# Kernel tuning notes

Hardware: AMD Instinct MI355X
Metric: run time of the kernel (lower is better)

Reference implementation:

```python
import jax, jax.numpy as jnp
import numpy as np
import math

D = 768
H = 8
DH = D // H
T = 4
MODES = 16
NUM_CLASSES = 14


def setup_inputs() -> dict:
    key = jax.random.key(0)
    ks = iter(jax.random.split(key, 64))
    B, S = 256, 512
    inp = {}
    inp['x_feat'] = jax.random.normal(next(ks), (B, S, D), dtype=jnp.float32)
    # attention pool
    inp['pool_w'] = jax.random.normal(next(ks), (D, 1), dtype=jnp.float32) * 0.02
    inp['pool_b'] = jnp.zeros((1,), dtype=jnp.float32)
    # per-block params, stacked over T
    def pstack(shape, scale=0.02):
        return jax.random.normal(next(ks), (T,) + shape, dtype=jnp.float32) * scale
    inp['w_q'] = pstack((D, D)); inp['w_k'] = pstack((D, D)); inp['w_v'] = pstack((D, D))
    inp['b_qkv'] = jnp.zeros((T, 3 * D), dtype=jnp.float32)
    inp['w_o'] = pstack((D, D)); inp['b_o'] = jnp.zeros((T, D), dtype=jnp.float32)
    inp['ln1_g'] = jnp.ones((T, D), dtype=jnp.float32); inp['ln1_b'] = jnp.zeros((T, D), dtype=jnp.float32)
    inp['ln2_g'] = jnp.ones((T, D), dtype=jnp.float32); inp['ln2_b'] = jnp.zeros((T, D), dtype=jnp.float32)
    inp['scale_real'] = pstack((MODES, D)); inp['scale_imag'] = pstack((MODES, D))
    inp['proj_w'] = pstack((D, D)); inp['proj_b'] = jnp.zeros((T, D), dtype=jnp.float32)
    inp['bn_g'] = jnp.ones((T, D), dtype=jnp.float32); inp['bn_b'] = jnp.zeros((T, D), dtype=jnp.float32)
    inp['gate'] = jnp.full((T,), 0.5, dtype=jnp.float32)
    inp['scale_attn'] = jnp.ones((T,), dtype=jnp.float32)
    inp['scale_denoise'] = jnp.ones((T,), dtype=jnp.float32)
    # fuse MLP + classifier
    inp['f1_w'] = jax.random.normal(next(ks), (D, 256), dtype=jnp.float32) * 0.02
    inp['f1_b'] = jnp.zeros((256,), dtype=jnp.float32)
    inp['f1_bn_g'] = jnp.ones((256,), dtype=jnp.float32); inp['f1_bn_b'] = jnp.zeros((256,), dtype=jnp.float32)
    inp['f2_w'] = jax.random.normal(next(ks), (256, 128), dtype=jnp.float32) * 0.02
    inp['f2_b'] = jnp.zeros((128,), dtype=jnp.float32)
    inp['f2_bn_g'] = jnp.ones((128,), dtype=jnp.float32); inp['f2_bn_b'] = jnp.zeros((128,), dtype=jnp.float32)
    inp['cls_w'] = jax.random.normal(next(ks), (128, NUM_CLASSES), dtype=jnp.float32) * 0.02
    inp['cls_b'] = jnp.zeros((NUM_CLASSES,), dtype=jnp.float32)
    return inp


def _layernorm(x, g, b, eps=1e-5):
    mu = jnp.mean(x, axis=-1, keepdims=True)
    var = jnp.var(x, axis=-1, keepdims=True)
    return (x - mu) * jax.lax.rsqrt(var + eps) * g + b


def _bn_eval(x, g, b, eps=1e-5):
    # eval-mode BatchNorm1d with running_mean=0, running_var=1
    return x * (g / jnp.sqrt(1.0 + eps)) + b


def _forward(x_feat, pool_w, pool_b, w_q, w_k, w_v, b_qkv, w_o, b_o,
             ln1_g, ln1_b, ln2_g, ln2_b, scale_real, scale_imag, proj_w, proj_b,
             bn_g, bn_b, gate, scale_attn, scale_denoise,
             f1_w, f1_b, f1_bn_g, f1_bn_b, f2_w, f2_b, f2_bn_g, f2_bn_b,
             cls_w, cls_b):
    B, S, _ = x_feat.shape
    # attention pool: softmax over seq of a scalar score per token
    scores = x_feat @ pool_w + pool_b          # [B,S,1]
    weights = jax.nn.softmax(scores, axis=1)
    z = jnp.sum(weights * x_feat, axis=1)      # [B,D]

    def classify(z):
        h = jax.nn.relu(_bn_eval(z @ f1_w + f1_b, f1_bn_g, f1_bn_b))
        h = jax.nn.relu(_bn_eval(h @ f2_w + f2_b, f2_bn_g, f2_bn_b))
        return h @ cls_w + cls_b

    logits_sum = jnp.zeros((B, NUM_CLASSES), dtype=x_feat.dtype)
    for t in range(T):
        bq, bk, bv = b_qkv[t, :D], b_qkv[t, D:2 * D], b_qkv[t, 2 * D:]
        # query: single token z [B,1,D]; keys/values: x_feat [B,S,D]
        q = (z @ w_q[t].T + bq).reshape(B, H, 1, DH)
        k = (x_feat @ w_k[t].T + bk).reshape(B, S, H, DH).transpose(0, 2, 1, 3)
        v = (x_feat @ w_v[t].T + bv).reshape(B, S, H, DH).transpose(0, 2, 1, 3)
        att = jax.nn.softmax(jnp.einsum('bhqd,bhsd->bhqs', q, k) / math.sqrt(DH), axis=-1)
        o = jnp.einsum('bhqs,bhsd->bhqd', att, v).reshape(B, D)
        z_attn = o @ w_o[t].T + b_o[t]
        z1 = _layernorm(z + scale_attn[t] * z_attn, ln1_g[t], ln1_b[t])
        # fft denoise: keep first MODES freq bins scaled by mean of complex filter per mode
        z_freq = jnp.fft.fft(z1, axis=1)                        # [B,D] complex
        filt = jnp.mean(scale_real[t] + 1j * scale_imag[t], axis=1)  # [MODES] complex
        keep = z_freq[:, :MODES] * filt[None, :]
        z_filtered = jnp.concatenate([keep, jnp.zeros((B, D - MODES), dtype=z_freq.dtype)], axis=1)
        z_spatial = jnp.fft.ifft(z_filtered, axis=1).real
        z_den = z_spatial @ proj_w[t].T + proj_b[t]
        z2 = _layernorm(z1 + scale_denoise[t] * z_den, ln2_g[t], ln2_b[t])
        g = jax.nn.sigmoid(gate[t])
        z3 = g * z2 + (1.0 - g) * z
        z = _bn_eval(z3, bn_g[t], bn_b[t])
        logits_sum = logits_sum + classify(z)
    return logits_sum / T


def reference(x_feat, pool_w, pool_b, w_q, w_k, w_v, b_qkv, w_o, b_o,
              ln1_g, ln1_b, ln2_g, ln2_b, scale_real, scale_imag, proj_w, proj_b,
              bn_g, bn_b, gate, scale_attn, scale_denoise,
              f1_w, f1_b, f1_bn_g, f1_bn_b, f2_w, f2_b, f2_bn_g, f2_bn_b,
              cls_w, cls_b):
    return _forward(x_feat, pool_w, pool_b, w_q, w_k, w_v, b_qkv, w_o, b_o,
                    ln1_g, ln1_b, ln2_g, ln2_b, scale_real, scale_imag, proj_w, proj_b,
                    bn_g, bn_b, gate, scale_attn, scale_denoise,
                    f1_w, f1_b, f1_bn_g, f1_bn_b, f2_w, f2_b, f2_bn_g, f2_bn_b,
                    cls_w, cls_b)
```

## Files before the change

### kernel.cpp

```cpp
#include <hip/hip_runtime.h>
#include <math.h>


#define DEV __device__ __forceinline__

typedef unsigned int   uint32;
typedef unsigned short ushort_t;
typedef __attribute__((ext_vector_type(8))) short bf16x8;
typedef __attribute__((ext_vector_type(4))) float f32x4;
typedef __attribute__((ext_vector_type(2))) float f32x2;

constexpr int Bv  = 256;
constexpr int Sv  = 512;
constexpr int Dv  = 768;
constexpr int Hv  = 8;
constexpr int DHv = 96;
constexpr int NCv = 14;

constexpr size_t ZL  = 196608;
constexpr size_t XWL = 1572864;
constexpr size_t WL  = 2359296;
constexpr size_t WT  = 589824;

DEV float4 ld4(const float* p) { return *reinterpret_cast<const float4*>(p); }

DEV ushort_t f2bf(float f) {
    uint32 u = __float_as_uint(f);
    u += 0x7FFFu + ((u >> 16) & 1u);
    return (ushort_t)(u >> 16);
}
DEV float bf2f(ushort_t h) { return __uint_as_float((uint32)h << 16); }
DEV void split2(float f, ushort_t& hi, ushort_t& lo) {
    hi = f2bf(f);
    lo = f2bf(f - bf2f(hi));
}
DEV uint2 pack4(float4 v) {
    return make_uint2((uint32)f2bf(v.x) | ((uint32)f2bf(v.y) << 16),
                      (uint32)f2bf(v.z) | ((uint32)f2bf(v.w) << 16));
}

DEV f32x2 bfpair(uint32 u) {
    f32x2 r;
    r.x = __uint_as_float(u << 16);
    r.y = __uint_as_float(u & 0xFFFF0000u);
    return r;
}

DEV f32x2 pkfma(f32x2 a, f32x2 b, f32x2 c) {
    f32x2 d;
    asm("v_pk_fma_f32 %0, %1, %2, %3" : "=v"(d) : "v"(a), "v"(b), "v"(c));
    return d;
}

DEV void glds16(const void* g, void* l) {
    __builtin_amdgcn_global_load_lds(
        (const __attribute__((address_space(1))) void*)g,
        (__attribute__((address_space(3))) void*)l, 16, 0, 0);
}

__global__ __launch_bounds__(512, 4)
void pool_cvt_kernel(const float* __restrict__ x, const float* __restrict__ pool_w,
                     ushort_t* __restrict__ xbf,
                     float* __restrict__ pacc, float2* __restrict__ pml)
{
    __shared__ float qks[Dv];
    const int b = blockIdx.x, half = blockIdx.y;
    const int tid = threadIdx.x, wave = tid >> 6, lane = tid & 63;
    for (int i = tid; i < Dv / 4; i += 512)
        *reinterpret_cast<float4*>(&qks[i * 4]) = ld4(pool_w + i * 4);
    __syncthreads();

    const int row0 = half * 256 + wave * 32;
    const float* base = x + ((size_t)b * Sv + row0) * Dv + 4 * lane;

    float4 acc[3];
#pragma unroll
    for (int j = 0; j < 3; ++j) acc[j] = make_float4(0.f, 0.f, 0.f, 0.f);
    float m = -INFINITY, l = 0.f;

    float4 c0[3], c1[3];
#pragma unroll
    for (int j = 0; j < 3; ++j) { c0[j] = ld4(base + 256 * j); c1[j] = ld4(base + Dv + 256 * j); }

    for (int it = 0; it < 16; ++it) {
        float4 n0_[3], n1_[3];
        if (it < 15) {
            const float* nb = base + (size_t)(2 * it + 2) * Dv;
#pragma unroll
            for (int j = 0; j < 3; ++j) { n0_[j] = ld4(nb + 256 * j); n1_[j] = ld4(nb + Dv + 256 * j); }
        }
        ushort_t* ob = xbf + ((size_t)b * Sv + row0 + 2 * it) * Dv + 4 * lane;
#pragma unroll
        for (int j = 0; j < 3; ++j) *reinterpret_cast<uint2*>(ob + 256 * j) = pack4(c0[j]);
#pragma unroll
        for (int j = 0; j < 3; ++j) *reinterpret_cast<uint2*>(ob + Dv + 256 * j) = pack4(c1[j]);
        float p0 = 0.f, p1 = 0.f;
#pragma unroll
        for (int j = 0; j < 3; ++j) {
            const float4 q4 = *reinterpret_cast<const float4*>(&qks[4 * lane + 256 * j]);
            p0 = fmaf(q4.x, c0[j].x, p0); p0 = fmaf(q4.y, c0[j].y, p0);
            p0 = fmaf(q4.z, c0[j].z, p0); p0 = fmaf(q4.w, c0[j].w, p0);
            p1 = fmaf(q4.x, c1[j].x, p1); p1 = fmaf(q4.y, c1[j].y, p1);
            p1 = fmaf(q4.z, c1[j].z, p1); p1 = fmaf(q4.w, c1[j].w, p1);
        }
#pragma unroll
        for (int dd = 1; dd < 64; dd <<= 1) { p0 += __shfl_xor(p0, dd); p1 += __shfl_xor(p1, dd); }
        float mx = fmaxf(p0, p1);
        if (mx > m) {
            float r = __expf(m - mx); l *= r;
#pragma unroll
            for (int j = 0; j < 3; ++j) { acc[j].x *= r; acc[j].y *= r; acc[j].z *= r; acc[j].w *= r; }
            m = mx;
        }
        float w0 = __expf(p0 - m), w1 = __expf(p1 - m);
        l += w0 + w1;
#pragma unroll
        for (int j = 0; j < 3; ++j) {
            acc[j].x = fmaf(w1, c1[j].x, fmaf(w0, c0[j].x, acc[j].x));
            acc[j].y = fmaf(w1, c1[j].y, fmaf(w0, c0[j].y, acc[j].y));
            acc[j].z = fmaf(w1, c1[j].z, fmaf(w0, c0[j].z, acc[j].z));
            acc[j].w = fmaf(w1, c1[j].w, fmaf(w0, c0[j].w, acc[j].w));
        }
        if (it < 15) {
#pragma unroll
            for (int j = 0; j < 3; ++j) { c0[j] = n0_[j]; c1[j] = n1_[j]; }
        }
    }
    const int p = half * 8 + wave;
    const size_t pidx = (size_t)p * 256 + b;
#pragma unroll
    for (int j = 0; j < 3; ++j)
        *reinterpret_cast<float4*>(&pacc[pidx * Dv + 4 * lane + 256 * j]) = acc[j];
    if (lane == 0) pml[pidx] = make_float2(m, l);
}

__global__ __launch_bounds__(512, 4)
void attn_flash_kernel(const ushort_t* __restrict__ xbf, const float* __restrict__ Qk,
                       float* __restrict__ pacc, float2* __restrict__ pml, float scale)
{
    const int b = blockIdx.x, half = blockIdx.y;
    const int tid = threadIdx.x, wave = tid >> 6, lane = tid & 63;
    const int hg = wave & 3, slice = wave >> 2;
    const int h0 = 2 * hg, h1 = h0 + 1;
    const int row0 = half * 256 + slice * 128;

    f32x2 q0[6], q1[6];
    {
        const float* qp0 = Qk + ((size_t)b * Hv + h0) * Dv + 4 * lane;
        const float* qp1 = Qk + ((size_t)b * Hv + h1) * Dv + 4 * lane;
#pragma unroll
        for (int s = 0; s < 3; ++s) {
            float4 a = ld4(qp0 + s * 256);
            float4 c = ld4(qp1 + s * 256);
            q0[2 * s]     = (f32x2){a.x, a.y}; q0[2 * s + 1] = (f32x2){a.z, a.w};
            q1[2 * s]     = (f32x2){c.x, c.y}; q1[2 * s + 1] = (f32x2){c.z, c.w};
        }
    }
    f32x2 a0[6], a1[6];
#pragma unroll
    for (int c = 0; c < 6; ++c) { a0[c] = (f32x2){0.f, 0.f}; a1[c] = (f32x2){0.f, 0.f}; }
    float m0 = -INFINITY, l0 = 0.f, m1 = -INFINITY, l1 = 0.f;

    const ushort_t* base = xbf + ((size_t)b * Sv + row0) * Dv + 4 * lane;

    uint2 c0[3], c1[3];
#pragma unroll
    for (int s = 0; s < 3; ++s) {
        c0[s] = *reinterpret_cast<const uint2*>(base + s * 256);
        c1[s] = *reinterpret_cast<const uint2*>(base + Dv + s * 256);
    }

    for (int it = 0; it < 64; ++it) {
        uint2 n0[3], n1[3];
        if (it < 63) {
            const ushort_t* nb = base + (size_t)(2 * it + 2) * Dv;
#pragma unroll
            for (int s = 0; s < 3; ++s) {
                n0[s] = *reinterpret_cast<const uint2*>(nb + s * 256);
                n1[s] = *reinterpret_cast<const uint2*>(nb + Dv + s * 256);
            }
        }
        f32x2 xf0[6], xf1[6];
#pragma unroll
        for (int s = 0; s < 3; ++s) {
            xf0[2 * s] = bfpair(c0[s].x); xf0[2 * s + 1] = bfpair(c0[s].y);
            xf1[2 * s] = bfpair(c1[s].x); xf1[2 * s + 1] = bfpair(c1[s].y);
        }
        f32x2 t00 = (f32x2){0.f, 0.f}, t01 = t00, t10 = t00, t11 = t00;
#pragma unroll
        for (int c = 0; c < 6; ++c) {
            t00 = pkfma(xf0[c], q0[c], t00);
            t01 = pkfma(xf0[c], q1[c], t01);
            t10 = pkfma(xf1[c], q0[c], t10);
            t11 = pkfma(xf1[c], q1[c], t11);
        }
        float s4[4];
        s4[0] = t00.x + t00.y;
        s4[1] = t01.x + t01.y;
        s4[2] = t10.x + t10.y;
        s4[3] = t11.x + t11.y;
        {
            const bool k0 = (lane & 1), k1 = (lane & 2);
            float sd0 = k0 ? s4[0] : s4[1];
            float rc0 = __shfl_xor(sd0, 1);
            float t0  = (k0 ? s4[1] : s4[0]) + rc0;
            float sd1 = k0 ? s4[2] : s4[3];
            float rc1 = __shfl_xor(sd1, 1);
            float t1  = (k0 ? s4[3] : s4[2]) + rc1;
            float sd2 = k1 ? t0 : t1;
            float rc2 = __shfl_xor(sd2, 2);
            float u   = (k1 ? t1 : t0) + rc2;
            u += __shfl_xor(u, 4);  u += __shfl_xor(u, 8);
            u += __shfl_xor(u, 16); u += __shfl_xor(u, 32);
            float b1 = __shfl_xor(u, 1);
            float b2 = __shfl_xor(u, 2);
            float b3 = __shfl_xor(u, 3);
            s4[0] = k1 ? (k0 ? b3 : b2) : (k0 ? b1 : u);
            s4[1] = k1 ? (k0 ? b2 : b3) : (k0 ? u  : b1);
            s4[2] = k1 ? (k0 ? b1 : u ) : (k0 ? b3 : b2);
            s4[3] = k1 ? (k0 ? u  : b1) : (k0 ? b2 : b3);
        }
#pragma unroll
        for (int j = 0; j < 4; ++j) s4[j] *= scale;
        {
            float mx = fmaxf(s4[0], s4[2]);
            if (mx > m0) {
                float f = __expf(m0 - mx); l0 *= f;
#pragma unroll
                for (int c = 0; c < 6; ++c) { a0[c].x *= f; a0[c].y *= f; }
                m0 = mx;
            }
            float w0 = __expf(s4[0] - m0), w1 = __expf(s4[2] - m0);
            l0 += w0 + w1;
            f32x2 w02 = (f32x2){w0, w0}, w12 = (f32x2){w1, w1};
#pragma unroll
            for (int c = 0; c < 6; ++c) a0[c] = pkfma(xf1[c], w12, pkfma(xf0[c], w02, a0[c]));
        }
        {
            float mx = fmaxf(s4[1], s4[3]);
            if (mx > m1) {
                float f = __expf(m1 - mx); l1 *= f;
#pragma unroll
                for (int c = 0; c < 6; ++c) { a1[c].x *= f; a1[c].y *= f; }
                m1 = mx;
            }
            float w0 = __expf(s4[1] - m1), w1 = __expf(s4[3] - m1);
            l1 += w0 + w1;
            f32x2 w02 = (f32x2){w0, w0}, w12 = (f32x2){w1, w1};
#pragma unroll
            for (int c = 0; c < 6; ++c) a1[c] = pkfma(xf1[c], w12, pkfma(xf0[c], w02, a1[c]));
        }
        if (it < 63) {
#pragma unroll
            for (int s = 0; s < 3; ++s) { c0[s] = n0[s]; c1[s] = n1[s]; }
        }
    }

    const int p = half * 2 + slice;
    const size_t pidx0 = ((size_t)p * 256 + b) * Hv + h0;
    const size_t pidx1 = pidx0 + 1;
    float* pb0 = pacc + pidx0 * Dv + 4 * lane;
    float* pb1 = pacc + pidx1 * Dv + 4 * lane;
#pragma unroll
    for (int s = 0; s < 3; ++s) {
        *reinterpret_cast<float4*>(pb0 + s * 256) =
            make_float4(a0[2 * s].x, a0[2 * s].y, a0[2 * s + 1].x, a0[2 * s + 1].y);
        *reinterpret_cast<float4*>(pb1 + s * 256) =
            make_float4(a1[2 * s].x, a1[2 * s].y, a1[2 * s + 1].x, a1[2 * s + 1].y);
    }
    if (lane == 0) {
        pml[pidx0] = make_float2(m0, l0);
        pml[pidx1] = make_float2(m1, l1);
    }
}

template<int NH, int NP, bool WF32>
__global__ __launch_bounds__(256)
void merge_kernel(const float* __restrict__ pacc, const float2* __restrict__ pml,
                  ushort_t* __restrict__ obf, size_t loOff, float* __restrict__ of32)
{
    __shared__ float eS[NH * NP];
    const int b = blockIdx.x, tid = threadIdx.x;
    if (tid < NH) {
        float2 mls[NP];
        float mm = -INFINITY;
#pragma unroll
        for (int p = 0; p < NP; ++p) {
            mls[p] = pml[((size_t)p * 256 + b) * NH + tid];
            mm = fmaxf(mm, mls[p].x);
        }
        float ee[NP]; float L = 0.f;
#pragma unroll
        for (int p = 0; p < NP; ++p) { ee[p] = __expf(mls[p].x - mm); L += mls[p].y * ee[p]; }
        float inv = 1.f / L;
#pragma unroll
        for (int p = 0; p < NP; ++p) eS[tid * NP + p] = ee[p] * inv;
    }
    __syncthreads();
#pragma unroll
    for (int seg = 0; seg < NH * 3; ++seg) {
        int h = seg / 3;
        int d = (seg - h * 3) * 256 + tid;
        float v = 0.f;
#pragma unroll
        for (int p = 0; p < NP; ++p)
            v += pacc[((size_t)((size_t)p * 256 + b) * NH + h) * Dv + d] * eS[h * NP + p];
        size_t oi = ((size_t)b * NH + h) * Dv + d;
        ushort_t hi, lo; split2(v, hi, lo);
        obf[oi] = hi; obf[oi + loOff] = lo;
        if (WF32) of32[oi] = v;
    }
}

template<int MODE, bool OBF>
__global__ __launch_bounds__(256)
void mgemm_kernel(const ushort_t* __restrict__ A, size_t aLo,
                  const ushort_t* __restrict__ W, size_t wLo,
                  const float* __restrict__ bias, void* __restrict__ outp,
                  size_t oLo)
{
    constexpr int BN = (MODE == 2) ? 96 : 64;
    constexpr int BK = (MODE == 1) ? 32 : 64;
    constexpr int NJ = BN / 32;
    constexpr int KTOT = (MODE == 1) ? 96 : 768;
    constexpr int NSTEP = KTOT / BK;
    constexpr int CH = BK / 8;
    constexpr int CA = (64 * BK) / 512;
    constexpr int CB = (BN * BK) / 512;
    constexpr int NC = 2 * (CA + CB) / 4;
    constexpr int LDA = (MODE == 2) ? 6144 : 768;
    constexpr int LDW = (MODE == 1) ? 96 : 768;
    constexpr int LDO = (MODE == 1) ? 6144 : 768;
    constexpr int WCW = (MODE == 2) ? 48 : 32;
    constexpr int RSH = (BK == 64) ? 7 : 6;

    __shared__ ushort_t As[2][2][64 * BK];
    __shared__ ushort_t Bs[2][2][BN * BK];

    const int tid = threadIdx.x, wave = tid >> 6, lane = tid & 63;
    const int n0 = blockIdx.x * BN;
    const int m0 = blockIdx.y * 64;
    const int h  = (MODE == 1) ? blockIdx.z : ((MODE == 2) ? blockIdx.x : 0);
    const int acol = (MODE == 1) ? h * 96 : ((MODE == 2) ? h * 768 : 0);
    const ushort_t* Wb = W + ((MODE == 1) ? (size_t)h * 768 * 96 : (size_t)0);
    const int ocol = (MODE == 1) ? h * 768 : 0;

    const int wr = wave >> 1, wc = wave & 1;
    const int l15 = lane & 15, kg = lane >> 4;

    auto stage = [&](int kt, int buf) {
#pragma unroll
        for (int hl = 0; hl < 2; ++hl) {
            const ushort_t* Ap = A + (hl ? aLo : 0);
            const ushort_t* Wp = Wb + (hl ? wLo : 0);
#pragma unroll
            for (int c = 0; c < CA / 4; ++c) {
                int call = wave + 4 * c;
                int off = call * 1024 + lane * 16;
                int row = off >> RSH;
                int chunk = (off & (2 * BK - 1)) >> 4;
                int sw = chunk ^ (row & (CH - 1));
                const ushort_t* src = Ap + (size_t)(m0 + row) * LDA + acol + kt + sw * 8;
                glds16(src, (char*)As[buf][hl] + call * 1024);
            }
#pragma unroll
            for (int c = 0; c < CB / 4; ++c) {
                int call = wave + 4 * c;
                int off = call * 1024 + lane * 16;
                int row = off >> RSH;
                int chunk = (off & (2 * BK - 1)) >> 4;
                int sw = chunk ^ (row & (CH - 1));
                const ushort_t* src = Wp + (size_t)(n0 + row) * LDW + kt + sw * 8;
                glds16(src, (char*)Bs[buf][hl] + call * 1024);
            }
        }
    };

    f32x4 acc[2][NJ];
#pragma unroll
    for (int i = 0; i < 2; ++i)
#pragma unroll
        for (int j = 0; j < NJ; ++j) acc[i][j] = (f32x4){0.f, 0.f, 0.f, 0.f};

    stage(0, 0);
    int cur = 0;
    for (int s = 0; s < NSTEP; ++s) {
        __builtin_amdgcn_s_barrier();
        if (s + 1 < NSTEP) {
            stage((s + 1) * BK, cur ^ 1);
            asm volatile("s_waitcnt vmcnt(%0)" :: "i"(NC) : "memory");
        } else {
            asm volatile("s_waitcnt vmcnt(0)" ::: "memory");
        }
        __builtin_amdgcn_s_barrier();
        __builtin_amdgcn_sched_barrier(0);

        const ushort_t* ah_ = As[cur][0];
        const ushort_t* al_ = As[cur][1];
        const ushort_t* bh_ = Bs[cur][0];
        const ushort_t* bl_ = Bs[cur][1];
#pragma unroll
        for (int kw = 0; kw < BK / 32; ++kw) {
            const int kb = kw * 4;
            bf16x8 ah[2], al[2], bh[NJ], bl[NJ];
#pragma unroll
            for (int i = 0; i < 2; ++i) {
                int r = wr * 32 + i * 16 + l15;
                int c = (kb + kg) ^ (r & (CH - 1));
                ah[i] = *reinterpret_cast<const bf16x8*>(&ah_[r * BK + c * 8]);
                al[i] = *reinterpret_cast<const bf16x8*>(&al_[r * BK + c * 8]);
            }
#pragma unroll
            for (int j = 0; j < NJ; ++j) {
                int r = wc * WCW + j * 16 + l15;
                int c = (kb + kg) ^ (r & (CH - 1));
                bh[j] = *reinterpret_cast<const bf16x8*>(&bh_[r * BK + c * 8]);
                bl[j] = *reinterpret_cast<const bf16x8*>(&bl_[r * BK + c * 8]);
            }
#pragma unroll
            for (int i = 0; i < 2; ++i)
#pragma unroll
                for (int j = 0; j < NJ; ++j) {
                    acc[i][j] = __builtin_amdgcn_mfma_f32_16x16x32_bf16(al[i], bh[j], acc[i][j], 0, 0, 0);
                    acc[i][j] = __builtin_amdgcn_mfma_f32_16x16x32_bf16(ah[i], bl[j], acc[i][j], 0, 0, 0);
                    acc[i][j] = __builtin_amdgcn_mfma_f32_16x16x32_bf16(ah[i], bh[j], acc[i][j], 0, 0, 0);
                }
        }
        cur ^= 1;
    }

#pragma unroll
    for (int i = 0; i < 2; ++i)
#pragma unroll
        for (int j = 0; j < NJ; ++j) {
            int rg = m0 + wr * 32 + i * 16 + kg * 4;
            int cg = n0 + wc * WCW + j * 16 + l15;
            float bv = bias ? bias[cg] : 0.f;
#pragma unroll
            for (int reg = 0; reg < 4; ++reg) {
                float v = acc[i][j][reg] + bv;
                size_t oi = (size_t)(rg + reg) * LDO + ocol + cg;
                if (OBF) {
                    ushort_t hi, lo; split2(v, hi, lo);
                    ((ushort_t*)outp)[oi] = hi;
                    ((ushort_t*)outp)[oi + oLo] = lo;
                } else {
                    ((float*)outp)[oi] = v;
                }
            }
        }
}

__global__ __launch_bounds__(256)
void cvt3_kernel(const float* __restrict__ wq, const float* __restrict__ wv,
                 const float* __restrict__ wo, ushort_t* __restrict__ dst)
{
    const int bid = blockIdx.x;
    const int w = bid / 1152;
    const int off = (bid - w * 1152) * 2048 + threadIdx.x * 8;
    const float* src = (w == 0) ? wq : (w == 1) ? wv : wo;
    ushort_t hi[8], lo[8];
#pragma unroll
    for (int e = 0; e < 8; ++e) split2(src[off + e], hi[e], lo[e]);
    ushort_t* base = dst + (size_t)w * (2 * WL);
    *reinterpret_cast<uint4*>(base + off) = *reinterpret_cast<uint4*>(hi);
    *reinterpret_cast<uint4*>(base + WL + off) = *reinterpret_cast<uint4*>(lo);
}

__global__ __launch_bounds__(256)
void wkT_kernel(const float* __restrict__ w_k, ushort_t* __restrict__ wkT)
{
    __shared__ float tile[96][65];
    const int n0 = blockIdx.x * 64;
    const int th = blockIdx.y;
    const int t = th >> 3, h = th & 7;
    const float* src = w_k + ((size_t)t * Dv + h * DHv) * Dv + n0;
    for (int idx = threadIdx.x; idx < 96 * 64; idx += 256) {
        int j = idx >> 6, n = idx & 63;
        tile[j][n] = src[(size_t)j * Dv + n];
    }
    __syncthreads();
    for (int idx = threadIdx.x; idx < 64 * 96; idx += 256) {
        int n = idx / 96, j = idx - n * 96;
        ushort_t hi, lo; split2(tile[j][n], hi, lo);
        size_t oi = ((size_t)th * Dv + n0 + n) * DHv + j;
        wkT[oi] = hi; wkT[oi + WL] = lo;
    }
}

__global__ __launch_bounds__(256)
void pre1_kernel(float* __restrict__ twc, float* __restrict__ tws,
                 const float* __restrict__ sr, const float* __restrict__ si,
                 float* __restrict__ filt)
{
    __shared__ float red[8];
    const int bid = blockIdx.x;
    if (bid < 48) {
        int idx = bid * 256 + threadIdx.x;
        int k = idx / Dv, n = idx % Dv;
        int r = (k * n) % Dv;
        float ang = (float)r * (float)(6.283185307179586 / 768.0);
        twc[idx] = cosf(ang);
        tws[idx] = sinf(ang);
    } else {
        int tk = bid - 48;
        const float* a  = sr + (size_t)tk * Dv;
        const float* b2 = si + (size_t)tk * Dv;
        float s1 = 0.f, s2 = 0.f;
#pragma unroll
        for (int j = 0; j < 3; ++j) {
            int c = threadIdx.x + 256 * j;
            s1 += a[c]; s2 += b2[c];
        }
        int wave = threadIdx.x >> 6, lane = threadIdx.x & 63;
#pragma unroll
        for (int dd = 1; dd < 64; dd <<= 1) { s1 += __shfl_xor(s1, dd); s2 += __shfl_xor(s2, dd); }
        if (lane == 0) { red[wave * 2] = s1; red[wave * 2 + 1] = s2; }
        __syncthreads();
        if (threadIdx.x == 0) {
            filt[tk * 2]     = (red[0] + red[2] + red[4] + red[6]) * (1.f / 768.f);
            filt[tk * 2 + 1] = (red[1] + red[3] + red[5] + red[7]) * (1.f / 768.f);
        }
    }
}

__global__ __launch_bounds__(256)
void cs_kernel(const float* __restrict__ proj_w, const float* __restrict__ twc,
               const float* __restrict__ tws, float* __restrict__ csC,
               float* __restrict__ csS)
{
    const int wave = threadIdx.x >> 6, lane = threadIdx.x & 63;
    const int gw = blockIdx.x * 4 + wave;
    const int t = gw / 768;
    const int i = gw - t * 768;
    const float* pr = proj_w + ((size_t)t * Dv + i) * Dv + 4 * lane;
    float4 p4[3];
#pragma unroll
    for (int j = 0; j < 3; ++j) p4[j] = ld4(pr + 256 * j);
    for (int k = 0; k < 16; ++k) {
        const float* tc = twc + (size_t)k * Dv + 4 * lane;
        const float* ts = tws + (size_t)k * Dv + 4 * lane;
        float ac = 0.f, as = 0.f;
#pragma unroll
        for (int j = 0; j < 3; ++j) {
            float4 c4 = ld4(tc + 256 * j);
            float4 s4 = ld4(ts + 256 * j);
            ac = fmaf(p4[j].x, c4.x, ac); ac = fmaf(p4[j].y, c4.y, ac);
            ac = fmaf(p4[j].z, c4.z, ac); ac = fmaf(p4[j].w, c4.w, ac);
            as = fmaf(p4[j].x, s4.x, as); as = fmaf(p4[j].y, s4.y, as);
            as = fmaf(p4[j].z, s4.z, as); as = fmaf(p4[j].w, s4.w, as);
        }
#pragma unroll
        for (int dd = 1; dd < 64; dd <<= 1) {
            ac += __shfl_xor(ac, dd);
            as += __shfl_xor(as, dd);
        }
        if (lane == 0) {
            csC[((size_t)t * 16 + k) * Dv + i] = ac * (1.f / 768.f);
            csS[((size_t)t * 16 + k) * Dv + i] = as * (1.f / 768.f);
        }
    }
}

__global__ __launch_bounds__(256)
void lnden_kernel(float* __restrict__ z, ushort_t* __restrict__ zbf,
                  const float* __restrict__ za,
                  const float* __restrict__ g1, const float* __restrict__ b1,
                  const float* __restrict__ g2, const float* __restrict__ b2,
                  const float* __restrict__ bng, const float* __restrict__ bnb,
                  const float* __restrict__ gate_p, const float* __restrict__ sa_p,
                  const float* __restrict__ sd_p,
                  const float* __restrict__ twc, const float* __restrict__ tws,
                  const float* __restrict__ filt_t,
                  const float* __restrict__ csC_t, const float* __restrict__ csS_t,
                  const float* __restrict__ pb_t,
                  const float* __restrict__ f1w, const float* __restrict__ f1b,
                  const float* __restrict__ f1g, const float* __restrict__ f1bb,
                  const float* __restrict__ f2w, const float* __restrict__ f2b,
                  const float* __restrict__ f2g, const float* __restrict__ f2bb,
                  const float* __restrict__ clw, const float* __restrict__ clb,
                  float* __restrict__ outp, int t)
{
    const int b = blockIdx.x, tid = threadIdx.x;
    const int wave = tid >> 6, lane = tid & 63;
    __shared__ float red[8];
    __shared__ float dred[4][32];
    __shared__ float fin[32];
    __shared__ float kr[16], ki[16];
    __shared__ float zs[768];
    __shared__ float h1s[256];
    __shared__ float h2s[128];

    const float sa = sa_p[0];
    float v[3], zo[3];
    float s = 0.f, s2 = 0.f;
#pragma unroll
    for (int j = 0; j < 3; ++j) {
        int c = tid + 256 * j;
        zo[j] = z[(size_t)b * Dv + c];
        float val = zo[j] + sa * za[(size_t)b * Dv + c];
        v[j] = val; s += val; s2 += val * val;
    }
#pragma unroll
    for (int dd = 1; dd < 64; dd <<= 1) { s += __shfl_xor(s, dd); s2 += __shfl_xor(s2, dd); }
    if (lane == 0) { red[wave * 2] = s; red[wave * 2 + 1] = s2; }
    __syncthreads();
    {
        const float mean = (red[0] + red[2] + red[4] + red[6]) * (1.f / 768.f);
        const float var  = (red[1] + red[3] + red[5] + red[7]) * (1.f / 768.f) - mean * mean;
        const float rstd = rsqrtf(var + 1e-5f);
#pragma unroll
        for (int j = 0; j < 3; ++j) {
            int c = tid + 256 * j;
            v[j] = (v[j] - mean) * rstd * g1[c] + b1[c];
        }
    }
    float Fc[16], Fs[16];
#pragma unroll
    for (int k = 0; k < 16; ++k) { Fc[k] = 0.f; Fs[k] = 0.f; }
#pragma unroll
    for (int j = 0; j < 3; ++j) {
        int c = tid + 256 * j;
#pragma unroll
        for (int k = 0; k < 16; ++k) {
            Fc[k] = fmaf(v[j], twc[k * Dv + c], Fc[k]);
            Fs[k] = fmaf(v[j], tws[k * Dv + c], Fs[k]);
        }
    }
#pragma unroll
    for (int dd = 1; dd < 64; dd <<= 1) {
#pragma unroll
        for (int k = 0; k < 16; ++k) { Fc[k] += __shfl_xor(Fc[k], dd); Fs[k] += __shfl_xor(Fs[k], dd); }
    }
    if (lane == 0) {
#pragma unroll
        for (int k = 0; k < 16; ++k) { dred[wave][k] = Fc[k]; dred[wave][16 + k] = Fs[k]; }
    }
    __syncthreads();
    if (tid < 32) fin[tid] = dred[0][tid] + dred[1][tid] + dred[2][tid] + dred[3][tid];
    __syncthreads();
    if (tid < 16) {
        float Sc = fin[tid], Ss = fin[16 + tid];
        float fr = filt_t[tid * 2], fi = filt_t[tid * 2 + 1];
        kr[tid] = Sc * fr + Ss * fi;
        ki[tid] = Sc * fi - Ss * fr;
    }
    __syncthreads();

    const float sd  = sd_p[0];
    const float gv  = 1.f / (1.f + expf(-gate_p[0]));
    const float bnc = 1.f / sqrtf(1.f + 1e-5f);
    float w3[3];
    s = 0.f; s2 = 0.f;
#pragma unroll
    for (int j = 0; j < 3; ++j) {
        int c = tid + 256 * j;
        float den = pb_t[c];
#pragma unroll
        for (int k = 0; k < 16; ++k) {
            den = fmaf(kr[k], csC_t[k * Dv + c], den);
            den = fmaf(-ki[k], csS_t[k * Dv + c], den);
        }
        float val = v[j] + sd * den;
        w3[j] = val; s += val; s2 += val * val;
    }
#pragma unroll
    for (int dd = 1; dd < 64; dd <<= 1) { s += __shfl_xor(s, dd); s2 += __shfl_xor(s2, dd); }
    if (lane == 0) { red[wave * 2] = s; red[wave * 2 + 1] = s2; }
    __syncthreads();
    const float mean2 = (red[0] + red[2] + red[4] + red[6]) * (1.f / 768.f);
    const float var2  = (red[1] + red[3] + red[5] + red[7]) * (1.f / 768.f) - mean2 * mean2;
    const float rstd2 = rsqrtf(var2 + 1e-5f);
#pragma unroll
    for (int j = 0; j < 3; ++j) {
        int c = tid + 256 * j;
        float z2v = (w3[j] - mean2) * rstd2 * g2[c] + b2[c];
        float z3v = gv * z2v + (1.f - gv) * zo[j];
        float zn  = z3v * (bng[c] * bnc) + bnb[c];
        z[(size_t)b * Dv + c] = zn;
        ushort_t hi, lo; split2(zn, hi, lo);
        zbf[(size_t)b * Dv + c] = hi;
        zbf[(size_t)b * Dv + c + ZL] = lo;
        zs[c] = zn;
    }
    __syncthreads();
    float h = f1b[tid];
    for (int d = 0; d < 768; ++d) h = fmaf(zs[d], f1w[(size_t)d * 256 + tid], h);
    h = h * (f1g[tid] * bnc) + f1bb[tid];
    h1s[tid] = fmaxf(h, 0.f);
    __syncthreads();
    if (tid < 128) {
        float h2 = f2b[tid];
        for (int i2 = 0; i2 < 256; ++i2) h2 = fmaf(h1s[i2], f2w[(size_t)i2 * 128 + tid], h2);
        h2 = h2 * (f2g[tid] * bnc) + f2bb[tid];
        h2s[tid] = fmaxf(h2, 0.f);
    }
    __syncthreads();
    if (tid < NCv) {
        float lg = clb[tid];
        for (int i2 = 0; i2 < 128; ++i2) lg = fmaf(h2s[i2], clw[(size_t)i2 * NCv + tid], lg);
        lg *= 0.25f;
        if (t == 0) outp[(size_t)b * NCv + tid] = lg;
        else        outp[(size_t)b * NCv + tid] += lg;
    }
}

extern "C" void kernel_launch(void* const* d_in, const int* in_sizes, int n_in,
                              void* d_out, int out_size, void* d_ws, size_t ws_size,
                              hipStream_t stream)
{
    (void)in_sizes; (void)n_in; (void)out_size; (void)ws_size;
    const float* x      = (const float*)d_in[0];
    const float* pool_w = (const float*)d_in[1];
    const float* w_q   = (const float*)d_in[3];
    const float* w_k   = (const float*)d_in[4];
    const float* w_v   = (const float*)d_in[5];
    const float* b_qkv = (const float*)d_in[6];
    const float* w_o   = (const float*)d_in[7];
    const float* b_o   = (const float*)d_in[8];
    const float* ln1_g = (const float*)d_in[9];
    const float* ln1_b = (const float*)d_in[10];
    const float* ln2_g = (const float*)d_in[11];
    const float* ln2_b = (const float*)d_in[12];
    const float* s_re  = (const float*)d_in[13];
    const float* s_im  = (const float*)d_in[14];
    const float* proj_w= (const float*)d_in[15];
    const float* proj_b= (const float*)d_in[16];
    const float* bn_g  = (const float*)d_in[17];
    const float* bn_b  = (const float*)d_in[18];
    const float* gate  = (const float*)d_in[19];
    const float* s_at  = (const float*)d_in[20];
    const float* s_dn  = (const float*)d_in[21];
    const float* f1w   = (const float*)d_in[22];
    const float* f1b   = (const float*)d_in[23];
    const float* f1g   = (const float*)d_in[24];
    const float* f1bb  = (const float*)d_in[25];
    const float* f2w   = (const float*)d_in[26];
    const float* f2b   = (const float*)d_in[27];
    const float* f2g   = (const float*)d_in[28];
    const float* f2bb  = (const float*)d_in[29];
    const float* clw   = (const float*)d_in[30];
    const float* clb   = (const float*)d_in[31];
    float* out = (float*)d_out;

    float* ws   = (float*)d_ws;
    float* twc  = ws;
    float* tws  = twc + 12288;
    float* filt = tws + 12288;
    float* csC  = filt + 128;
    float* csS  = csC + 49152;
    float* z    = csS + 49152;
    float* za   = z + 196608;
    float* Qk   = za + 196608;
    float* pacc = Qk + 1572864;
    float* pmlf = pacc + 6291456;
    ushort_t* xbf  = (ushort_t*)(pmlf + 16384);
    ushort_t* zbf  = xbf + 100663296;
    ushort_t* qbf  = zbf + 2 * ZL;
    ushort_t* xwbf = qbf + 2 * ZL;
    ushort_t* obf  = xwbf + 2 * XWL;
    ushort_t* wspl = obf + 2 * ZL;
    ushort_t* wkT  = wspl + 6 * WL;
    float2* pml = (float2*)pmlf;
    ushort_t* wqbf = wspl;
    ushort_t* wvbf = wspl + 2 * WL;
    ushort_t* wobf = wspl + 4 * WL;

    pre1_kernel<<<112, 256, 0, stream>>>(twc, tws, s_re, s_im, filt);
    cs_kernel<<<768, 256, 0, stream>>>(proj_w, twc, tws, csC, csS);
    cvt3_kernel<<<3456, 256, 0, stream>>>(w_q, w_v, w_o, wspl);
    wkT_kernel<<<dim3(12, 32), 256, 0, stream>>>(w_k, wkT);

    pool_cvt_kernel<<<dim3(256, 2), 512, 0, stream>>>(x, pool_w, xbf, pacc, pml);
    merge_kernel<1, 16, true><<<256, 256, 0, stream>>>(pacc, pml, zbf, ZL, z);

    const float iscale = (float)(1.0 / sqrt(96.0));
    for (int t = 0; t < 4; ++t) {
        mgemm_kernel<0, true><<<dim3(12, 4), 256, 0, stream>>>(
            zbf, ZL, wqbf + (size_t)t * WT, WL, b_qkv + (size_t)t * 2304, qbf, ZL);
        mgemm_kernel<1, false><<<dim3(12, 4, 8), 256, 0, stream>>>(
            qbf, ZL, wkT + (size_t)t * WT, WL, nullptr, Qk, 0);
        attn_flash_kernel<<<dim3(256, 2), 512, 0, stream>>>(xbf, Qk, pacc, pml, iscale);
        merge_kernel<8, 4, false><<<256, 256, 0, stream>>>(pacc, pml, xwbf, XWL, nullptr);
        mgemm_kernel<2, true><<<dim3(8, 4), 256, 0, stream>>>(
            xwbf, XWL, wvbf + (size_t)t * WT, WL, b_qkv + (size_t)t * 2304 + 1536, obf, ZL);
        mgemm_kernel<0, false><<<dim3(12, 4), 256, 0, stream>>>(
            obf, ZL, wobf + (size_t)t * WT, WL, b_o + (size_t)t * Dv, za, 0);
        lnden_kernel<<<256, 256, 0, stream>>>(
            z, zbf, za,
            ln1_g + (size_t)t * Dv, ln1_b + (size_t)t * Dv,
            ln2_g + (size_t)t * Dv, ln2_b + (size_t)t * Dv,
            bn_g + (size_t)t * Dv, bn_b + (size_t)t * Dv,
            gate + t, s_at + t, s_dn + t,
            twc, tws, filt + (size_t)t * 32,
            csC + (size_t)t * 12288, csS + (size_t)t * 12288,
            proj_b + (size_t)t * Dv,
            f1w, f1b, f1g, f1bb, f2w, f2b, f2g, f2bb,
            clw, clb, out, t);
    }
}
```

Measured before the change: 930.9 us.

## Split fused flash attention into MFMA score GEMM, softmax, and PV passes

Replaces the single-pass online-softmax attention kernel with three stages: an MFMA bf16 GEMM computing scores from split hi/lo Qk against x, a separate softmax kernel writing bf16 probabilities, and a PV kernel doing only weighted accumulation, followed by a simple sum merge. The aim is to move the QK dot products off packed FMA onto matrix cores and remove the cross-lane shuffle reductions and rescaling from the inner loop. In exchange, x is read twice per step from memory, there are extra launches and intermediate buffers, and probabilities are rounded to bf16.

```diff
diff --git a/kernel.cpp b/kernel.cpp
--- a/kernel.cpp
+++ b/kernel.cpp
@@ -21,6 +21,7 @@
 constexpr size_t XWL = 1572864;
 constexpr size_t WL  = 2359296;
 constexpr size_t WT  = 589824;
+constexpr size_t QKL = 3145728;
 
 DEV float4 ld4(const float* p) { return *reinterpret_cast<const float4*>(p); }
 
@@ -134,146 +135,6 @@
     if (lane == 0) pml[pidx] = make_float2(m, l);
 }
 
-__global__ __launch_bounds__(512, 4)
-void attn_flash_kernel(const ushort_t* __restrict__ xbf, const float* __restrict__ Qk,
-                       float* __restrict__ pacc, float2* __restrict__ pml, float scale)
-{
-    const int b = blockIdx.x, half = blockIdx.y;
-    const int tid = threadIdx.x, wave = tid >> 6, lane = tid & 63;
-    const int hg = wave & 3, slice = wave >> 2;
-    const int h0 = 2 * hg, h1 = h0 + 1;
-    const int row0 = half * 256 + slice * 128;
-
-    f32x2 q0[6], q1[6];
-    {
-        const float* qp0 = Qk + ((size_t)b * Hv + h0) * Dv + 4 * lane;
-        const float* qp1 = Qk + ((size_t)b * Hv + h1) * Dv + 4 * lane;
-#pragma unroll
-        for (int s = 0; s < 3; ++s) {
-            float4 a = ld4(qp0 + s * 256);
-            float4 c = ld4(qp1 + s * 256);
-            q0[2 * s]     = (f32x2){a.x, a.y}; q0[2 * s + 1] = (f32x2){a.z, a.w};
-            q1[2 * s]     = (f32x2){c.x, c.y}; q1[2 * s + 1] = (f32x2){c.z, c.w};
-        }
-    }
-    f32x2 a0[6], a1[6];
-#pragma unroll
-    for (int c = 0; c < 6; ++c) { a0[c] = (f32x2){0.f, 0.f}; a1[c] = (f32x2){0.f, 0.f}; }
-    float m0 = -INFINITY, l0 = 0.f, m1 = -INFINITY, l1 = 0.f;
-
-    const ushort_t* base = xbf + ((size_t)b * Sv + row0) * Dv + 4 * lane;
-
-    uint2 c0[3], c1[3];
-#pragma unroll
-    for (int s = 0; s < 3; ++s) {
-        c0[s] = *reinterpret_cast<const uint2*>(base + s * 256);
-        c1[s] = *reinterpret_cast<const uint2*>(base + Dv + s * 256);
-    }
-
-    for (int it = 0; it < 64; ++it) {
-        uint2 n0[3], n1[3];
-        if (it < 63) {
-            const ushort_t* nb = base + (size_t)(2 * it + 2) * Dv;
-#pragma unroll
-            for (int s = 0; s < 3; ++s) {
-                n0[s] = *reinterpret_cast<const uint2*>(nb + s * 256);
-                n1[s] = *reinterpret_cast<const uint2*>(nb + Dv + s * 256);
-            }
-        }
-        f32x2 xf0[6], xf1[6];
-#pragma unroll
-        for (int s = 0; s < 3; ++s) {
-            xf0[2 * s] = bfpair(c0[s].x); xf0[2 * s + 1] = bfpair(c0[s].y);
-            xf1[2 * s] = bfpair(c1[s].x); xf1[2 * s + 1] = bfpair(c1[s].y);
-        }
-        f32x2 t00 = (f32x2){0.f, 0.f}, t01 = t00, t10 = t00, t11 = t00;
-#pragma unroll
-        for (int c = 0; c < 6; ++c) {
-            t00 = pkfma(xf0[c], q0[c], t00);
-            t01 = pkfma(xf0[c], q1[c], t01);
-            t10 = pkfma(xf1[c], q0[c], t10);
-            t11 = pkfma(xf1[c], q1[c], t11);
-        }
-        float s4[4];
-        s4[0] = t00.x + t00.y;
-        s4[1] = t01.x + t01.y;
-        s4[2] = t10.x + t10.y;
-        s4[3] = t11.x + t11.y;
-        {
-            const bool k0 = (lane & 1), k1 = (lane & 2);
-            float sd0 = k0 ? s4[0] : s4[1];
-            float rc0 = __shfl_xor(sd0, 1);
-            float t0  = (k0 ? s4[1] : s4[0]) + rc0;
-            float sd1 = k0 ? s4[2] : s4[3];
-            float rc1 = __shfl_xor(sd1, 1);
-            float t1  = (k0 ? s4[3] : s4[2]) + rc1;
-            float sd2 = k1 ? t0 : t1;
-            float rc2 = __shfl_xor(sd2, 2);
-            float u   = (k1 ? t1 : t0) + rc2;
-            u += __shfl_xor(u, 4);  u += __shfl_xor(u, 8);
-            u += __shfl_xor(u, 16); u += __shfl_xor(u, 32);
-            float b1 = __shfl_xor(u, 1);
-            float b2 = __shfl_xor(u, 2);
-            float b3 = __shfl_xor(u, 3);
-            s4[0] = k1 ? (k0 ? b3 : b2) : (k0 ? b1 : u);
-            s4[1] = k1 ? (k0 ? b2 : b3) : (k0 ? u  : b1);
-            s4[2] = k1 ? (k0 ? b1 : u ) : (k0 ? b3 : b2);
-            s4[3] = k1 ? (k0 ? u  : b1) : (k0 ? b2 : b3);
-        }
-#pragma unroll
-        for (int j = 0; j < 4; ++j) s4[j] *= scale;
-        {
-            float mx = fmaxf(s4[0], s4[2]);
-            if (mx > m0) {
-                float f = __expf(m0 - mx); l0 *= f;
-#pragma unroll
-                for (int c = 0; c < 6; ++c) { a0[c].x *= f; a0[c].y *= f; }
-                m0 = mx;
-            }
-            float w0 = __expf(s4[0] - m0), w1 = __expf(s4[2] - m0);
-            l0 += w0 + w1;
-            f32x2 w02 = (f32x2){w0, w0}, w12 = (f32x2){w1, w1};
-#pragma unroll
-            for (int c = 0; c < 6; ++c) a0[c] = pkfma(xf1[c], w12, pkfma(xf0[c], w02, a0[c]));
-        }
-        {
-            float mx = fmaxf(s4[1], s4[3]);
-            if (mx > m1) {
-                float f = __expf(m1 - mx); l1 *= f;
-#pragma unroll
-                for (int c = 0; c < 6; ++c) { a1[c].x *= f; a1[c].y *= f; }
-                m1 = mx;
-            }
-            float w0 = __expf(s4[1] - m1), w1 = __expf(s4[3] - m1);
-            l1 += w0 + w1;
-            f32x2 w02 = (f32x2){w0, w0}, w12 = (f32x2){w1, w1};
-#pragma unroll
-            for (int c = 0; c < 6; ++c) a1[c] = pkfma(xf1[c], w12, pkfma(xf0[c], w02, a1[c]));
-        }
-        if (it < 63) {
-#pragma unroll
-            for (int s = 0; s < 3; ++s) { c0[s] = n0[s]; c1[s] = n1[s]; }
-        }
-    }
-
-    const int p = half * 2 + slice;
-    const size_t pidx0 = ((size_t)p * 256 + b) * Hv + h0;
-    const size_t pidx1 = pidx0 + 1;
-    float* pb0 = pacc + pidx0 * Dv + 4 * lane;
-    float* pb1 = pacc + pidx1 * Dv + 4 * lane;
-#pragma unroll
-    for (int s = 0; s < 3; ++s) {
-        *reinterpret_cast<float4*>(pb0 + s * 256) =
-            make_float4(a0[2 * s].x, a0[2 * s].y, a0[2 * s + 1].x, a0[2 * s + 1].y);
-        *reinterpret_cast<float4*>(pb1 + s * 256) =
-            make_float4(a1[2 * s].x, a1[2 * s].y, a1[2 * s + 1].x, a1[2 * s + 1].y);
-    }
-    if (lane == 0) {
-        pml[pidx0] = make_float2(m0, l0);
-        pml[pidx1] = make_float2(m1, l1);
-    }
-}
-
 template<int NH, int NP, bool WF32>
 __global__ __launch_bounds__(256)
 void merge_kernel(const float* __restrict__ pacc, const float2* __restrict__ pml,
@@ -309,6 +170,215 @@
         ushort_t hi, lo; split2(v, hi, lo);
         obf[oi] = hi; obf[oi + loOff] = lo;
         if (WF32) of32[oi] = v;
+    }
+}
+
+__global__ __launch_bounds__(256)
+void sgemm_kernel(const ushort_t* __restrict__ qkbf,
+                  const ushort_t* __restrict__ xbf,
+                  float* __restrict__ S)
+{
+    __shared__ ushort_t As[2][2][16 * 64];
+    __shared__ ushort_t Ws[2][256 * 64];
+    const int tid = threadIdx.x, wave = tid >> 6, lane = tid & 63;
+    const int n0 = blockIdx.x * 256;
+    const int b  = blockIdx.y;
+    const int l15 = lane & 15, kg = lane >> 4;
+
+    auto stage = [&](int kt, int buf) {
+#pragma unroll
+        for (int c = 0; c < 9; ++c) {
+            int call = wave + 4 * c;
+            if (call < 4) {
+                int hl  = call >> 1;
+                int off = (call & 1) * 1024 + lane * 16;
+                int row = off >> 7;
+                int chunk = (off & 127) >> 4;
+                int sw  = chunk ^ (row & 7);
+                const ushort_t* src = qkbf + (hl ? QKL : 0) +
+                    ((size_t)b * 16 + row) * 768 + kt + sw * 8;
+                glds16(src, (char*)As[buf][hl] + off);
+            } else {
+                int wc  = call - 4;
+                int off = wc * 1024 + lane * 16;
+                int row = off >> 7;
+                int chunk = (off & 127) >> 4;
+                int sw  = chunk ^ (row & 7);
+                const ushort_t* src = xbf +
+                    ((size_t)b * Sv + n0 + row) * 768 + kt + sw * 8;
+                glds16(src, (char*)Ws[buf] + off);
+            }
+        }
+    };
+
+    f32x4 acc[4];
+#pragma unroll
+    for (int j = 0; j < 4; ++j) acc[j] = (f32x4){0.f, 0.f, 0.f, 0.f};
+
+    stage(0, 0);
+    int cur = 0;
+    for (int s = 0; s < 12; ++s) {
+        __builtin_amdgcn_s_barrier();
+        if (s + 1 < 12) {
+            stage((s + 1) * 64, cur ^ 1);
+            asm volatile("s_waitcnt vmcnt(9)" ::: "memory");
+        } else {
+            asm volatile("s_waitcnt vmcnt(0)" ::: "memory");
+        }
+        __builtin_amdgcn_s_barrier();
+        __builtin_amdgcn_sched_barrier(0);
+
+        const ushort_t* ah_ = As[cur][0];
+        const ushort_t* al_ = As[cur][1];
+        const ushort_t* ws_ = Ws[cur];
+#pragma unroll
+        for (int kw = 0; kw < 2; ++kw) {
+            const int kb = kw * 4;
+            const int ca = (kb + kg) ^ (l15 & 7);
+            bf16x8 ah = *reinterpret_cast<const bf16x8*>(&ah_[l15 * 64 + ca * 8]);
+            bf16x8 al = *reinterpret_cast<const bf16x8*>(&al_[l15 * 64 + ca * 8]);
+#pragma unroll
+            for (int j = 0; j < 4; ++j) {
+                int r = wave * 64 + j * 16 + l15;
+                int c = (kb + kg) ^ (r & 7);
+                bf16x8 bw = *reinterpret_cast<const bf16x8*>(&ws_[r * 64 + c * 8]);
+                acc[j] = __builtin_amdgcn_mfma_f32_16x16x32_bf16(al, bw, acc[j], 0, 0, 0);
+                acc[j] = __builtin_amdgcn_mfma_f32_16x16x32_bf16(ah, bw, acc[j], 0, 0, 0);
+            }
+        }
+        cur ^= 1;
+    }
+
+    if (kg < 2) {
+#pragma unroll
+        for (int j = 0; j < 4; ++j) {
+            int col = n0 + wave * 64 + j * 16 + l15;
+#pragma unroll
+            for (int reg = 0; reg < 4; ++reg) {
+                S[((size_t)b * 8 + kg * 4 + reg) * 512 + col] = acc[j][reg];
+            }
+        }
+    }
+}
+
+__global__ __launch_bounds__(256)
+void softmax_kernel(const float* __restrict__ S, ushort_t* __restrict__ P,
+                    float scale)
+{
+    const int b = blockIdx.x, tid = threadIdx.x;
+    const int wave = tid >> 6, lane = tid & 63;
+#pragma unroll
+    for (int hh = 0; hh < 2; ++hh) {
+        const int h = wave * 2 + hh;
+        const float* Sp = S + ((size_t)b * 8 + h) * 512 + 8 * lane;
+        float4 v0 = ld4(Sp), v1 = ld4(Sp + 4);
+        v0.x *= scale; v0.y *= scale; v0.z *= scale; v0.w *= scale;
+        v1.x *= scale; v1.y *= scale; v1.z *= scale; v1.w *= scale;
+        float mx = fmaxf(fmaxf(fmaxf(v0.x, v0.y), fmaxf(v0.z, v0.w)),
+                         fmaxf(fmaxf(v1.x, v1.y), fmaxf(v1.z, v1.w)));
+#pragma unroll
+        for (int dd = 1; dd < 64; dd <<= 1) mx = fmaxf(mx, __shfl_xor(mx, dd));
+        float e0 = __expf(v0.x - mx), e1 = __expf(v0.y - mx);
+        float e2 = __expf(v0.z - mx), e3 = __expf(v0.w - mx);
+        float e4 = __expf(v1.x - mx), e5 = __expf(v1.y - mx);
+        float e6 = __expf(v1.z - mx), e7 = __expf(v1.w - mx);
+        float sm = ((e0 + e1) + (e2 + e3)) + ((e4 + e5) + (e6 + e7));
+#pragma unroll
+        for (int dd = 1; dd < 64; dd <<= 1) sm += __shfl_xor(sm, dd);
+        float inv = 1.f / sm;
+        uint2 p0 = pack4(make_float4(e0 * inv, e1 * inv, e2 * inv, e3 * inv));
+        uint2 p1 = pack4(make_float4(e4 * inv, e5 * inv, e6 * inv, e7 * inv));
+        *reinterpret_cast<uint4*>(P + ((size_t)b * 8 + h) * 512 + 8 * lane) =
+            make_uint4(p0.x, p0.y, p1.x, p1.y);
+    }
+}
+
+__global__ __launch_bounds__(512, 4)
+void pv_kernel(const ushort_t* __restrict__ xbf, const ushort_t* __restrict__ P,
+               float* __restrict__ pacc)
+{
+    const int b = blockIdx.x, half = blockIdx.y;
+    const int tid = threadIdx.x, wave = tid >> 6, lane = tid & 63;
+    const int hg = wave & 3, slice = wave >> 2;
+    const int h0 = 2 * hg, h1 = h0 + 1;
+    const int row0 = half * 256 + slice * 128;
+
+    f32x2 a0[6], a1[6];
+#pragma unroll
+    for (int c = 0; c < 6; ++c) { a0[c] = (f32x2){0.f, 0.f}; a1[c] = (f32x2){0.f, 0.f}; }
+
+    const ushort_t* base = xbf + ((size_t)b * Sv + row0) * Dv + 4 * lane;
+    const ushort_t* P0 = P + ((size_t)b * 8 + h0) * 512 + row0;
+    const ushort_t* P1 = P + ((size_t)b * 8 + h1) * 512 + row0;
+
+    uint2 c0[3], c1[3];
+#pragma unroll
+    for (int s = 0; s < 3; ++s) {
+        c0[s] = *reinterpret_cast<const uint2*>(base + s * 256);
+        c1[s] = *reinterpret_cast<const uint2*>(base + Dv + s * 256);
+    }
+
+    for (int it = 0; it < 64; ++it) {
+        uint2 n0[3], n1[3];
+        if (it < 63) {
+            const ushort_t* nb = base + (size_t)(2 * it + 2) * Dv;
+#pragma unroll
+            for (int s = 0; s < 3; ++s) {
+                n0[s] = *reinterpret_cast<const uint2*>(nb + s * 256);
+                n1[s] = *reinterpret_cast<const uint2*>(nb + Dv + s * 256);
+            }
+        }
+        f32x2 pw0 = bfpair(*reinterpret_cast<const uint32*>(P0 + 2 * it));
+        f32x2 pw1 = bfpair(*reinterpret_cast<const uint32*>(P1 + 2 * it));
+        f32x2 w00 = (f32x2){pw0.x, pw0.x}, w01 = (f32x2){pw0.y, pw0.y};
+        f32x2 w10 = (f32x2){pw1.x, pw1.x}, w11 = (f32x2){pw1.y, pw1.y};
+        f32x2 xf0[6], xf1[6];
+#pragma unroll
+        for (int s = 0; s < 3; ++s) {
+            xf0[2 * s] = bfpair(c0[s].x); xf0[2 * s + 1] = bfpair(c0[s].y);
+            xf1[2 * s] = bfpair(c1[s].x); xf1[2 * s + 1] = bfpair(c1[s].y);
+        }
+#pragma unroll
+        for (int c = 0; c < 6; ++c) {
+            a0[c] = pkfma(xf1[c], w01, pkfma(xf0[c], w00, a0[c]));
+            a1[c] = pkfma(xf1[c], w11, pkfma(xf0[c], w10, a1[c]));
+        }
+        if (it < 63) {
+#pragma unroll
+            for (int s = 0; s < 3; ++s) { c0[s] = n0[s]; c1[s] = n1[s]; }
+        }
+    }
+
+    const int p = half * 2 + slice;
+    const size_t pidx0 = ((size_t)p * 256 + b) * 8 + h0;
+    const size_t pidx1 = pidx0 + 1;
+    float* pb0 = pacc + pidx0 * Dv + 4 * lane;
+    float* pb1 = pacc + pidx1 * Dv + 4 * lane;
+#pragma unroll
+    for (int s = 0; s < 3; ++s) {
+        *reinterpret_cast<float4*>(pb0 + s * 256) =
+            make_float4(a0[2 * s].x, a0[2 * s].y, a0[2 * s + 1].x, a0[2 * s + 1].y);
+        *reinterpret_cast<float4*>(pb1 + s * 256) =
+            make_float4(a1[2 * s].x, a1[2 * s].y, a1[2 * s + 1].x, a1[2 * s + 1].y);
+    }
+}
+
+__global__ __launch_bounds__(256)
+void merge_sum_kernel(const float* __restrict__ pacc, ushort_t* __restrict__ obf,
+                      size_t loOff)
+{
+    const int b = blockIdx.x, tid = threadIdx.x;
+#pragma unroll
+    for (int seg = 0; seg < 24; ++seg) {
+        int h = seg / 3;
+        int d = (seg - h * 3) * 256 + tid;
+        float v = 0.f;
+#pragma unroll
+        for (int p = 0; p < 4; ++p)
+            v += pacc[((size_t)((size_t)p * 256 + b) * 8 + h) * Dv + d];
+        size_t oi = ((size_t)b * 8 + h) * Dv + d;
+        ushort_t hi, lo; split2(v, hi, lo);
+        obf[oi] = hi; obf[oi + loOff] = lo;
     }
 }
 
@@ -330,7 +400,7 @@
     constexpr int NC = 2 * (CA + CB) / 4;
     constexpr int LDA = (MODE == 2) ? 6144 : 768;
     constexpr int LDW = (MODE == 1) ? 96 : 768;
-    constexpr int LDO = (MODE == 1) ? 6144 : 768;
+    constexpr int LDO = (MODE == 1) ? 12288 : 768;
     constexpr int WCW = (MODE == 2) ? 48 : 32;
     constexpr int RSH = (BK == 64) ? 7 : 6;
 
@@ -751,8 +821,8 @@
     float* csS  = csC + 49152;
     float* z    = csS + 49152;
     float* za   = z + 196608;
-    float* Qk   = za + 196608;
-    float* pacc = Qk + 1572864;
+    float* Sm   = za + 196608;
+    float* pacc = Sm + 1048576;
     float* pmlf = pacc + 6291456;
     ushort_t* xbf  = (ushort_t*)(pmlf + 16384);
     ushort_t* zbf  = xbf + 100663296;
@@ -761,6 +831,8 @@
     ushort_t* obf  = xwbf + 2 * XWL;
     ushort_t* wspl = obf + 2 * ZL;
     ushort_t* wkT  = wspl + 6 * WL;
+    ushort_t* qkbf = wkT + 2 * WL;
+    ushort_t* Pbuf = qkbf + 2 * QKL;
     float2* pml = (float2*)pmlf;
     ushort_t* wqbf = wspl;
     ushort_t* wvbf = wspl + 2 * WL;
@@ -778,10 +850,12 @@
     for (int t = 0; t < 4; ++t) {
         mgemm_kernel<0, true><<<dim3(12, 4), 256, 0, stream>>>(
             zbf, ZL, wqbf + (size_t)t * WT, WL, b_qkv + (size_t)t * 2304, qbf, ZL);
-        mgemm_kernel<1, false><<<dim3(12, 4, 8), 256, 0, stream>>>(
-            qbf, ZL, wkT + (size_t)t * WT, WL, nullptr, Qk, 0);
-        attn_flash_kernel<<<dim3(256, 2), 512, 0, stream>>>(xbf, Qk, pacc, pml, iscale);
-        merge_kernel<8, 4, false><<<256, 256, 0, stream>>>(pacc, pml, xwbf, XWL, nullptr);
+        mgemm_kernel<1, true><<<dim3(12, 4, 8), 256, 0, stream>>>(
+            qbf, ZL, wkT + (size_t)t * WT, WL, nullptr, qkbf, QKL);
+        sgemm_kernel<<<dim3(2, 256), 256, 0, stream>>>(qkbf, xbf, Sm);
+        softmax_kernel<<<256, 256, 0, stream>>>(Sm, Pbuf, iscale);
+        pv_kernel<<<dim3(256, 2), 512, 0, stream>>>(xbf, Pbuf, pacc);
+        merge_sum_kernel<<<256, 256, 0, stream>>>(pacc, xwbf, XWL);
         mgemm_kernel<2, true><<<dim3(8, 4), 256, 0, stream>>>(
             xwbf, XWL, wvbf + (size_t)t * WT, WL, b_qkv + (size_t)t * 2304 + 1536, obf, ZL);
         mgemm_kernel<0, false><<<dim3(12, 4), 256, 0, stream>>>(
```

Result: slower. 983.5 us (+5.6%).
